# Kernel tuning notes

Hardware: AMD Instinct MI355X
Metric: run time of the kernel (lower is better)

Reference implementation:

```python
import jax, jax.numpy as jnp
import numpy as np

N = 6000          # number of nodes
P = 8_000_000     # number of (src, dst) pairs that have a path
D_FEAT = 128      # node feature dim (unused by the math, only shape)
MAX_PATH_DISTANCE = 5


def setup_inputs() -> dict:
    key = jax.random.key(0)
    k_x, k_b, k_s, k_d, k_l = jax.random.split(key, 5)
    x = jax.random.normal(k_x, (N, D_FEAT), dtype=jnp.float32)
    b = jax.random.normal(k_b, (MAX_PATH_DISTANCE,), dtype=jnp.float32)
    src_idx = jax.random.randint(k_s, (P,), 0, N, dtype=jnp.int64 if jax.config.jax_enable_x64 else jnp.int32)
    dst_idx = jax.random.randint(k_d, (P,), 0, N, dtype=src_idx.dtype)
    # path lengths are >= 1 (a path in the dict always has at least one node)
    path_len = jax.random.randint(k_l, (P,), 1, 21, dtype=src_idx.dtype)
    return {"x": x, "b": b, "src_idx": src_idx, "dst_idx": dst_idx, "path_len": path_len}


def reference(x, b, src_idx, dst_idx, path_len):
    # spatial_matrix[src, dst] = b[min(len(path), max_path_distance) - 1]
    n = x.shape[0]
    max_pd = b.shape[0]
    clamped = jnp.minimum(path_len, max_pd) - 1          # [P] in [0, max_pd-1]
    vals = b[clamped]                                     # gather from bias, [P]
    spatial = jnp.zeros((n, n), dtype=x.dtype)
    spatial = spatial.at[src_idx, dst_idx].set(vals)      # scatter into pairwise matrix
    return spatial
```

## Files before the change

kernel.cpp:

```cpp
#include <hip/hip_runtime.h>


#define BSHIFT 14
#define BCELLS (1 << BSHIFT)
#define NBUCK  2198
#define NPACK  1100
#define NOWN   550
#define BIN_THREADS 1024
#define TILE   12288
#define SCAN_TB 16
#define MAXBLK 656
#define MRG_THREADS 1024

__device__ __forceinline__ unsigned int unpack16(const unsigned int* A, unsigned int c) {
    return (A[c >> 1] >> ((c & 1) * 16)) & 0xFFFFu;
}


__global__ __launch_bounds__(BIN_THREADS, 8) void se_bin_local(
        const int* __restrict__ src_idx,
        const int* __restrict__ dst_idx,
        const int* __restrict__ path_len,
        unsigned int* __restrict__ recs,
        unsigned int* __restrict__ startsW,
        int P, int n) {
    __shared__ unsigned int histP[NPACK];
    __shared__ unsigned int curP[NPACK];
    __shared__ unsigned int stage[TILE];
    __shared__ unsigned int scr[34];

    int t = threadIdx.x;
    int start = blockIdx.x * TILE;

    for (int i = t; i < NPACK; i += BIN_THREADS) curP[i] = 0u;
    __syncthreads();

    unsigned int cc[12];
    unsigned int rk[6];
#pragma unroll
    for (int j = 0; j < 3; ++j) {
        int base = start + j * (BIN_THREADS * 4) + t * 4;
        int k0 = j * 4;
        if (base + 3 < P) {
            int4 s = *reinterpret_cast<const int4*>(src_idx + base);
            int4 d = *reinterpret_cast<const int4*>(dst_idx + base);
            int4 l = *reinterpret_cast<const int4*>(path_len + base);
            cc[k0]     = ((unsigned int)(s.x * n + d.x) << 3) | (unsigned int)((l.x < 5 ? l.x : 5) - 1);
            cc[k0 + 1] = ((unsigned int)(s.y * n + d.y) << 3) | (unsigned int)((l.y < 5 ? l.y : 5) - 1);
            cc[k0 + 2] = ((unsigned int)(s.z * n + d.z) << 3) | (unsigned int)((l.z < 5 ? l.z : 5) - 1);
            cc[k0 + 3] = ((unsigned int)(s.w * n + d.w) << 3) | (unsigned int)((l.w < 5 ? l.w : 5) - 1);
        } else {
#pragma unroll
            for (int jj = 0; jj < 4; ++jj) {
                int p = base + jj;
                if (p < P) {
                    int len = path_len[p];
                    cc[k0 + jj] = ((unsigned int)(src_idx[p] * n + dst_idx[p]) << 3)
                                | (unsigned int)((len < 5 ? len : 5) - 1);
                } else {
                    cc[k0 + jj] = 0xFFFFFFFFu;
                }
            }
        }
    }
#pragma unroll
    for (int k = 0; k < 12; ++k) {
        unsigned int r = 0;
        if (cc[k] != 0xFFFFFFFFu) {
            unsigned int c = cc[k] >> 17;
            unsigned int old = atomicAdd(&curP[c >> 1], (c & 1) ? 0x10000u : 1u);
            r = (old >> ((c & 1) * 16)) & 0xFFFFu;
        }
        if (k & 1) rk[k >> 1] |= r << 16; else rk[k >> 1] = r;
    }
    __syncthreads();

    unsigned int l0 = 0, l1 = 0, l2v = 0, l3 = 0, s = 0;
    if (t < NOWN) {
        unsigned int w0 = curP[2 * t], w1 = curP[2 * t + 1];
        unsigned int v0 = w0 & 0xFFFFu, v1 = w0 >> 16;
        unsigned int v2 = w1 & 0xFFFFu, v3 = w1 >> 16;
        l0 = 0; l1 = v0; l2v = v0 + v1; l3 = v0 + v1 + v2;
        s = v0 + v1 + v2 + v3;
    }
    unsigned int x = s;
    for (int d = 1; d < 64; d <<= 1) {
        unsigned int y = (unsigned int)__shfl_up((int)x, d, 64);
        if ((t & 63) >= d) x += y;
    }
    if ((t & 63) == 63) scr[t >> 6] = x;
    __syncthreads();
    if (t == 0) {
        unsigned int acc = 0;
        for (int w = 0; w < 16; ++w) { unsigned int v = scr[w]; scr[16 + w] = acc; acc += v; }
        scr[32] = acc;
    }
    __syncthreads();
    unsigned int exc = x - s + scr[16 + (t >> 6)];
    if (t < NOWN) {
        unsigned int st0 = exc + l0, st1 = exc + l1, st2 = exc + l2v, st3 = exc + l3;
        histP[2 * t]     = (st0 & 0xFFFFu) | (st1 << 16);
        histP[2 * t + 1] = (st2 & 0xFFFFu) | (st3 << 16);
    }
    __syncthreads();

    for (int i = t; i < NPACK; i += BIN_THREADS)
        startsW[(size_t)blockIdx.x * NPACK + i] = histP[i];

#pragma unroll
    for (int k = 0; k < 12; ++k) {
        if (cc[k] != 0xFFFFFFFFu) {
            unsigned int c = cc[k] >> 17;
            unsigned int rank = (rk[k >> 1] >> ((k & 1) * 16)) & 0xFFFFu;
            unsigned int pos = unpack16(histP, c) + rank;
            unsigned int lp1 = (unsigned int)((k >> 2) * (BIN_THREADS * 4) + t * 4 + (k & 3) + 1);
            stage[pos] = (((cc[k] >> 3) & (BCELLS - 1)) << 18) | (lp1 << 3) | (cc[k] & 7u);
        }
    }
    __syncthreads();

    unsigned int tot = scr[32];
    unsigned int* dst = recs + (size_t)blockIdx.x * TILE;
    const uint4* st4 = reinterpret_cast<const uint4*>(stage);
    uint4* dst4 = reinterpret_cast<uint4*>(dst);
    if (tot == TILE) {
#pragma unroll
        for (int j = 0; j < TILE / 4 / BIN_THREADS; ++j)
            dst4[j * BIN_THREADS + t] = st4[j * BIN_THREADS + t];
    } else {
        unsigned int tot4 = tot >> 2;
        for (unsigned int i = t; i < tot4; i += BIN_THREADS)
            dst4[i] = st4[i];
        for (unsigned int i = (tot4 << 2) + t; i < tot; i += BIN_THREADS)
            dst[i] = stage[i];
    }
}

__device__ __forceinline__ float se_decode(unsigned int k,
                                           float b0, float b1, float b2,
                                           float b3, float b4) {
    unsigned c = k & 7u;
    float t = (c == 0u) ? b0 : (c == 1u) ? b1 : (c == 2u) ? b2 : (c == 3u) ? b3 : b4;
    return k ? t : 0.0f;
}

__global__ __launch_bounds__(MRG_THREADS, 8) void se_merge3(
        const unsigned int* __restrict__ startsW,
        const unsigned int* __restrict__ recs,
        const float* __restrict__ b,
        float* __restrict__ out,
        long long totalCells, int nblk) {
    __shared__ unsigned int tab[BCELLS];

    int orig = blockIdx.x;
    int q = gridDim.x >> 3, r8 = gridDim.x & 7;
    int xcd = orig & 7, idx = orig >> 3;
    int c = (xcd < r8 ? xcd * (q + 1) : r8 * (q + 1) + (xcd - r8) * q) + idx;

    long long baseCell = (long long)c << BSHIFT;
    long long rem = totalCells - baseCell;
    int valid = rem < BCELLS ? (int)rem : BCELLS;

    int tr = threadIdx.x;
    unsigned int st = 0, en = 0;
    if (tr < nblk) {
        const unsigned int* sw = startsW + (size_t)tr * NPACK;
        unsigned int w0 = sw[c >> 1];
        unsigned int w1 = sw[(c + 1) >> 1];
        st = (w0 >> ((c & 1) * 16)) & 0xFFFFu;
        en = (w1 >> (((c + 1) & 1) * 16)) & 0xFFFFu;
    }

    uint4* tab4 = reinterpret_cast<uint4*>(tab);
    for (int i = threadIdx.x; i < BCELLS / 4; i += MRG_THREADS)
        tab4[i] = make_uint4(0u, 0u, 0u, 0u);
    __syncthreads();

    if (tr < nblk) {
        const uint4* rp4 =
            reinterpret_cast<const uint4*>(recs + (size_t)tr * TILE);
        unsigned int keyhi = (unsigned int)tr << 18;
        for (unsigned int i = st & ~3u; i < en; i += 4) {
            uint4 r4 = rp4[i >> 2];
            if (i     >= st && i     < en) atomicMax(&tab[r4.x >> 18], keyhi | (r4.x & 0x3FFFFu));
            if (i + 1 >= st && i + 1 < en) atomicMax(&tab[r4.y >> 18], keyhi | (r4.y & 0x3FFFFu));
            if (i + 2 >= st && i + 2 < en) atomicMax(&tab[r4.z >> 18], keyhi | (r4.z & 0x3FFFFu));
            if (i + 3 >= st && i + 3 < en) atomicMax(&tab[r4.w >> 18], keyhi | (r4.w & 0x3FFFFu));
        }
    }
    __syncthreads();

    float b0 = b[0], b1 = b[1], b2 = b[2], b3 = b[3], b4 = b[4];
    float* o = out + baseCell;
    int n4 = valid >> 2;
    float4* o4 = reinterpret_cast<float4*>(o);
    for (int i = threadIdx.x; i < n4; i += MRG_THREADS) {
        uint4 k = tab4[i];
        float4 v;
        v.x = se_decode(k.x, b0, b1, b2, b3, b4);
        v.y = se_decode(k.y, b0, b1, b2, b3, b4);
        v.z = se_decode(k.z, b0, b1, b2, b3, b4);
        v.w = se_decode(k.w, b0, b1, b2, b3, b4);
        o4[i] = v;
    }
    for (int i = (n4 << 2) + threadIdx.x; i < valid; i += MRG_THREADS)
        o[i] = se_decode(tab[i], b0, b1, b2, b3, b4);
}


__global__ __launch_bounds__(BIN_THREADS) void se_hist(
        const int* __restrict__ src_idx,
        const int* __restrict__ dst_idx,
        unsigned int* __restrict__ countsW,
        int P, int n) {
    __shared__ unsigned int curP[NPACK];
    int t = threadIdx.x;
    for (int i = t; i < NPACK; i += BIN_THREADS) curP[i] = 0u;
    __syncthreads();

    int start = blockIdx.x * TILE;
#pragma unroll
    for (int j = 0; j < 3; ++j) {
        int base = start + j * (BIN_THREADS * 4) + t * 4;
        if (base + 3 < P) {
            int4 s = *reinterpret_cast<const int4*>(src_idx + base);
            int4 d = *reinterpret_cast<const int4*>(dst_idx + base);
            unsigned int c0 = (unsigned int)(s.x * n + d.x) >> BSHIFT;
            unsigned int c1 = (unsigned int)(s.y * n + d.y) >> BSHIFT;
            unsigned int c2 = (unsigned int)(s.z * n + d.z) >> BSHIFT;
            unsigned int c3 = (unsigned int)(s.w * n + d.w) >> BSHIFT;
            atomicAdd(&curP[c0 >> 1], (c0 & 1) ? 0x10000u : 1u);
            atomicAdd(&curP[c1 >> 1], (c1 & 1) ? 0x10000u : 1u);
            atomicAdd(&curP[c2 >> 1], (c2 & 1) ? 0x10000u : 1u);
            atomicAdd(&curP[c3 >> 1], (c3 & 1) ? 0x10000u : 1u);
        } else {
            for (int p = base; p < P && p < base + 4; ++p) {
                unsigned int c = (unsigned int)(src_idx[p] * n + dst_idx[p]) >> BSHIFT;
                atomicAdd(&curP[c >> 1], (c & 1) ? 0x10000u : 1u);
            }
        }
    }
    __syncthreads();
    for (int i = t; i < NPACK; i += BIN_THREADS)
        countsW[(size_t)blockIdx.x * NPACK + i] = curP[i];
}

__global__ __launch_bounds__(256) void se_scan(
        unsigned int* __restrict__ countsW,
        unsigned short* __restrict__ basesT,
        int nblk) {
    __shared__ unsigned short lds16[MAXBLK * SCAN_TB];
    unsigned int* lds32 = reinterpret_cast<unsigned int*>(lds16);
    int t = threadIdx.x;
    int c0 = blockIdx.x * SCAN_TB;
    int w0 = c0 >> 1;
    int words = nblk * (SCAN_TB / 2);

    for (int i = t; i < words; i += 256) {
        int r = i >> 3, w = i & 7;
        if (w0 + w < NPACK)
            lds32[r * 8 + w] = countsW[(size_t)r * NPACK + w0 + w];
    }
    __syncthreads();

    if (t < SCAN_TB && c0 + t < NBUCK) {
        unsigned int acc = 0;
        for (int r = 0; r < nblk; ++r) {
            unsigned short v = lds16[r * SCAN_TB + t];
            lds16[r * SCAN_TB + t] = (unsigned short)acc;
            acc += v;
        }
        basesT[(size_t)(c0 + t) * (nblk + 1) + nblk] = (unsigned short)acc;
    }
    __syncthreads();

    for (int i = t; i < words; i += 256) {
        int r = i >> 3, w = i & 7;
        if (w0 + w < NPACK)
            countsW[(size_t)r * NPACK + w0 + w] = lds32[r * 8 + w];
    }
    for (int k = 0; k < SCAN_TB; ++k) {
        int c = c0 + k;
        if (c >= NBUCK) break;
        for (int r = t; r < nblk; r += 256)
            basesT[(size_t)c * (nblk + 1) + r] = lds16[r * SCAN_TB + k];
    }
}

__global__ __launch_bounds__(BIN_THREADS) void se_bin5(
        const int* __restrict__ src_idx,
        const int* __restrict__ dst_idx,
        const int* __restrict__ path_len,
        unsigned int* __restrict__ recs,
        const unsigned int* __restrict__ basesW,
        int P, int n) {
    __shared__ unsigned int histP[NPACK];
    __shared__ unsigned int curP[NPACK];
    __shared__ unsigned int gbaseP[NPACK];
    __shared__ unsigned int stage[TILE];
    __shared__ unsigned int scr[34];

    int t = threadIdx.x;
    int start = blockIdx.x * TILE;

    for (int i = t; i < NPACK; i += BIN_THREADS) curP[i] = 0u;
    __syncthreads();

    int cells[12];
    unsigned int lows[12];
#pragma unroll
    for (int j = 0; j < 3; ++j) {
        int base = start + j * (BIN_THREADS * 4) + t * 4;
        int k0 = j * 4;
        if (base + 3 < P) {
            int4 s = *reinterpret_cast<const int4*>(src_idx + base);
            int4 d = *reinterpret_cast<const int4*>(dst_idx + base);
            int4 l = *reinterpret_cast<const int4*>(path_len + base);
            int lp = base - start;
            cells[k0]     = s.x * n + d.x;
            cells[k0 + 1] = s.y * n + d.y;
            cells[k0 + 2] = s.z * n + d.z;
            cells[k0 + 3] = s.w * n + d.w;
            lows[k0]     = ((unsigned int)(lp + 1) << 3) | (unsigned int)((l.x < 5 ? l.x : 5) - 1);
            lows[k0 + 1] = ((unsigned int)(lp + 2) << 3) | (unsigned int)((l.y < 5 ? l.y : 5) - 1);
            lows[k0 + 2] = ((unsigned int)(lp + 3) << 3) | (unsigned int)((l.z < 5 ? l.z : 5) - 1);
            lows[k0 + 3] = ((unsigned int)(lp + 4) << 3) | (unsigned int)((l.w < 5 ? l.w : 5) - 1);
        } else {
#pragma unroll
            for (int jj = 0; jj < 4; ++jj) {
                int p = base + jj;
                if (p < P) {
                    cells[k0 + jj] = src_idx[p] * n + dst_idx[p];
                    int len = path_len[p];
                    int cl = (len < 5 ? len : 5) - 1;
                    lows[k0 + jj] = ((unsigned int)(p - start + 1) << 3) | (unsigned int)cl;
                } else {
                    cells[k0 + jj] = -1;
                    lows[k0 + jj] = 0u;
                }
            }
        }
    }
#pragma unroll
    for (int k = 0; k < 12; ++k) {
        if (cells[k] >= 0) {
            unsigned int c = (unsigned int)cells[k] >> BSHIFT;
            atomicAdd(&curP[c >> 1], (c & 1) ? 0x10000u : 1u);
        }
    }
    __syncthreads();

    unsigned int l0 = 0, l1 = 0, l2v = 0, l3 = 0, s = 0;
    if (t < NOWN) {
        unsigned int w0 = curP[2 * t], w1 = curP[2 * t + 1];
        unsigned int v0 = w0 & 0xFFFFu, v1 = w0 >> 16;
        unsigned int v2 = w1 & 0xFFFFu, v3 = w1 >> 16;
        l0 = 0; l1 = v0; l2v = v0 + v1; l3 = v0 + v1 + v2;
        s = v0 + v1 + v2 + v3;
    }
    unsigned int x = s;
    for (int d = 1; d < 64; d <<= 1) {
        unsigned int y = (unsigned int)__shfl_up((int)x, d, 64);
        if ((t & 63) >= d) x += y;
    }
    if ((t & 63) == 63) scr[t >> 6] = x;
    __syncthreads();
    if (t == 0) {
        unsigned int acc = 0;
        for (int w = 0; w < 16; ++w) { unsigned int v = scr[w]; scr[16 + w] = acc; acc += v; }
        scr[32] = acc;
    }
    __syncthreads();
    unsigned int exc = x - s + scr[16 + (t >> 6)];
    if (t < NOWN) {
        unsigned int st0 = exc + l0, st1 = exc + l1, st2 = exc + l2v, st3 = exc + l3;
        histP[2 * t]     = (st0 & 0xFFFFu) | (st1 << 16);
        histP[2 * t + 1] = (st2 & 0xFFFFu) | (st3 << 16);
    }
    __syncthreads();

    for (int i = t; i < NPACK; i += BIN_THREADS) {
        gbaseP[i] = basesW[(size_t)blockIdx.x * NPACK + i];
        curP[i] = histP[i];
    }
    __syncthreads();

#pragma unroll
    for (int k = 0; k < 12; ++k) {
        if (cells[k] >= 0) {
            unsigned int cell = (unsigned int)cells[k];
            unsigned int c = cell >> BSHIFT;
            unsigned int old = atomicAdd(&curP[c >> 1], (c & 1) ? 0x10000u : 1u);
            unsigned int pos = (old >> ((c & 1) * 16)) & 0xFFFFu;
            stage[pos] = ((cell & (BCELLS - 1)) << 18) | lows[k];
        }
    }
    __syncthreads();

    unsigned int tot = scr[32];
    for (unsigned int i = t; i < tot; i += BIN_THREADS) {
        unsigned int rec = stage[i];
        unsigned int lo = 0, hi = 2199;
        while (lo < hi) {
            unsigned int mid = (lo + hi + 1) >> 1;
            if (unpack16(histP, mid) <= i) lo = mid; else hi = mid - 1;
        }
        unsigned int c = lo;
        unsigned int pos = unpack16(gbaseP, c) + (i - unpack16(histP, c));
        recs[(size_t)c * BCELLS + pos] = rec;
    }
}

__global__ __launch_bounds__(MRG_THREADS) void se_merge(
        const unsigned short* __restrict__ basesT,
        const float* __restrict__ b,
        float* __restrict__ out,
        long long totalCells, int nblk) {
    __shared__ unsigned int tab[BCELLS];

    int c = blockIdx.x;
    long long baseCell = (long long)c << BSHIFT;
    long long rem = totalCells - baseCell;
    int valid = rem < BCELLS ? (int)rem : BCELLS;

    uint4* tab4 = reinterpret_cast<uint4*>(tab);
    for (int i = threadIdx.x; i < BCELLS / 4; i += MRG_THREADS)
        tab4[i] = make_uint4(0u, 0u, 0u, 0u);
    __syncthreads();

    const unsigned int* r =
        reinterpret_cast<const unsigned int*>(out) + (size_t)c * BCELLS;
    int tr = threadIdx.x;
    if (tr < nblk) {
        const unsigned short* B = basesT + (size_t)c * (nblk + 1);
        unsigned int rb0 = B[tr], rb1 = B[tr + 1];
        unsigned int keyhi = (unsigned int)tr << 18;
        for (unsigned int i = rb0; i < rb1; ++i) {
            unsigned int rec = r[i];
            atomicMax(&tab[rec >> 18], keyhi | (rec & 0x3FFFFu));
        }
    }
    __syncthreads();

    float b0 = b[0], b1 = b[1], b2 = b[2], b3 = b[3], b4 = b[4];
    float* o = out + baseCell;
    int n4 = valid >> 2;
    float4* o4 = reinterpret_cast<float4*>(o);
    for (int i = threadIdx.x; i < n4; i += MRG_THREADS) {
        uint4 k = tab4[i];
        float4 v;
        v.x = se_decode(k.x, b0, b1, b2, b3, b4);
        v.y = se_decode(k.y, b0, b1, b2, b3, b4);
        v.z = se_decode(k.z, b0, b1, b2, b3, b4);
        v.w = se_decode(k.w, b0, b1, b2, b3, b4);
        o4[i] = v;
    }
    for (int i = (n4 << 2) + threadIdx.x; i < valid; i += MRG_THREADS)
        o[i] = se_decode(tab[i], b0, b1, b2, b3, b4);
}


extern "C" void kernel_launch(void* const* d_in, const int* in_sizes, int n_in,
                              void* d_out, int out_size, void* d_ws, size_t ws_size,
                              hipStream_t stream) {
    const float* b        = (const float*)d_in[1];
    const int*   src_idx  = (const int*)d_in[2];
    const int*   dst_idx  = (const int*)d_in[3];
    const int*   path_len = (const int*)d_in[4];
    int P = in_sizes[2];
    int n = in_sizes[0] / 128;
    long long totalCells = (long long)n * n;
    int nblk = (P + TILE - 1) / TILE;

    size_t needFast = (size_t)nblk * TILE * 4u
                    + (size_t)nblk * NPACK * 4u;

    if (ws_size >= needFast && nblk <= MRG_THREADS) {
        unsigned int* recs    = (unsigned int*)d_ws;
        unsigned int* startsW = recs + (size_t)nblk * TILE;

        se_bin_local<<<nblk, BIN_THREADS, 0, stream>>>(
            src_idx, dst_idx, path_len, recs, startsW, P, n);

        se_merge3<<<NBUCK, MRG_THREADS, 0, stream>>>(
            startsW, recs, b, (float*)d_out, totalCells, nblk);
    } else {
        unsigned int*   countsW = (unsigned int*)d_ws;
        unsigned short* basesT  = (unsigned short*)(countsW + (size_t)nblk * NPACK);

        se_hist<<<nblk, BIN_THREADS, 0, stream>>>(src_idx, dst_idx, countsW, P, n);
        se_scan<<<(NBUCK + SCAN_TB - 1) / SCAN_TB, 256, 0, stream>>>(countsW, basesT, nblk);
        se_bin5<<<nblk, BIN_THREADS, 0, stream>>>(
            src_idx, dst_idx, path_len, (unsigned int*)d_out, countsW, P, n);
        se_merge<<<NBUCK, MRG_THREADS, 0, stream>>>(basesT, b, (float*)d_out,
                                                    totalCells, nblk);
    }
}
```

Measured before the change: 257.6 us.

## Fuse bin and merge kernels into one persistent kernel with grid barrier

Replaces the two-kernel bin/merge pipeline with a single persistent kernel of 512 blocks. Each block processes a strided range of input tiles, then all blocks meet at a software grid barrier (atomic counter plus spin-sleep), and each block then merges a contiguous range of output buckets. The aim is to remove the second kernel launch and the tail of the first grid. The cost is a spin barrier that relies on all 512 blocks being co-resident, an extra memset launch, and coarser work distribution per block.

```diff
diff --git a/kernel.cpp b/kernel.cpp
--- a/kernel.cpp
+++ b/kernel.cpp
@@ -11,129 +11,10 @@
 #define SCAN_TB 16
 #define MAXBLK 656
 #define MRG_THREADS 1024
+#define FUSED_GRID 512
 
 __device__ __forceinline__ unsigned int unpack16(const unsigned int* A, unsigned int c) {
     return (A[c >> 1] >> ((c & 1) * 16)) & 0xFFFFu;
-}
-
-
-__global__ __launch_bounds__(BIN_THREADS, 8) void se_bin_local(
-        const int* __restrict__ src_idx,
-        const int* __restrict__ dst_idx,
-        const int* __restrict__ path_len,
-        unsigned int* __restrict__ recs,
-        unsigned int* __restrict__ startsW,
-        int P, int n) {
-    __shared__ unsigned int histP[NPACK];
-    __shared__ unsigned int curP[NPACK];
-    __shared__ unsigned int stage[TILE];
-    __shared__ unsigned int scr[34];
-
-    int t = threadIdx.x;
-    int start = blockIdx.x * TILE;
-
-    for (int i = t; i < NPACK; i += BIN_THREADS) curP[i] = 0u;
-    __syncthreads();
-
-    unsigned int cc[12];
-    unsigned int rk[6];
-#pragma unroll
-    for (int j = 0; j < 3; ++j) {
-        int base = start + j * (BIN_THREADS * 4) + t * 4;
-        int k0 = j * 4;
-        if (base + 3 < P) {
-            int4 s = *reinterpret_cast<const int4*>(src_idx + base);
-            int4 d = *reinterpret_cast<const int4*>(dst_idx + base);
-            int4 l = *reinterpret_cast<const int4*>(path_len + base);
-            cc[k0]     = ((unsigned int)(s.x * n + d.x) << 3) | (unsigned int)((l.x < 5 ? l.x : 5) - 1);
-            cc[k0 + 1] = ((unsigned int)(s.y * n + d.y) << 3) | (unsigned int)((l.y < 5 ? l.y : 5) - 1);
-            cc[k0 + 2] = ((unsigned int)(s.z * n + d.z) << 3) | (unsigned int)((l.z < 5 ? l.z : 5) - 1);
-            cc[k0 + 3] = ((unsigned int)(s.w * n + d.w) << 3) | (unsigned int)((l.w < 5 ? l.w : 5) - 1);
-        } else {
-#pragma unroll
-            for (int jj = 0; jj < 4; ++jj) {
-                int p = base + jj;
-                if (p < P) {
-                    int len = path_len[p];
-                    cc[k0 + jj] = ((unsigned int)(src_idx[p] * n + dst_idx[p]) << 3)
-                                | (unsigned int)((len < 5 ? len : 5) - 1);
-                } else {
-                    cc[k0 + jj] = 0xFFFFFFFFu;
-                }
-            }
-        }
-    }
-#pragma unroll
-    for (int k = 0; k < 12; ++k) {
-        unsigned int r = 0;
-        if (cc[k] != 0xFFFFFFFFu) {
-            unsigned int c = cc[k] >> 17;
-            unsigned int old = atomicAdd(&curP[c >> 1], (c & 1) ? 0x10000u : 1u);
-            r = (old >> ((c & 1) * 16)) & 0xFFFFu;
-        }
-        if (k & 1) rk[k >> 1] |= r << 16; else rk[k >> 1] = r;
-    }
-    __syncthreads();
-
-    unsigned int l0 = 0, l1 = 0, l2v = 0, l3 = 0, s = 0;
-    if (t < NOWN) {
-        unsigned int w0 = curP[2 * t], w1 = curP[2 * t + 1];
-        unsigned int v0 = w0 & 0xFFFFu, v1 = w0 >> 16;
-        unsigned int v2 = w1 & 0xFFFFu, v3 = w1 >> 16;
-        l0 = 0; l1 = v0; l2v = v0 + v1; l3 = v0 + v1 + v2;
-        s = v0 + v1 + v2 + v3;
-    }
-    unsigned int x = s;
-    for (int d = 1; d < 64; d <<= 1) {
-        unsigned int y = (unsigned int)__shfl_up((int)x, d, 64);
-        if ((t & 63) >= d) x += y;
-    }
-    if ((t & 63) == 63) scr[t >> 6] = x;
-    __syncthreads();
-    if (t == 0) {
-        unsigned int acc = 0;
-        for (int w = 0; w < 16; ++w) { unsigned int v = scr[w]; scr[16 + w] = acc; acc += v; }
-        scr[32] = acc;
-    }
-    __syncthreads();
-    unsigned int exc = x - s + scr[16 + (t >> 6)];
-    if (t < NOWN) {
-        unsigned int st0 = exc + l0, st1 = exc + l1, st2 = exc + l2v, st3 = exc + l3;
-        histP[2 * t]     = (st0 & 0xFFFFu) | (st1 << 16);
-        histP[2 * t + 1] = (st2 & 0xFFFFu) | (st3 << 16);
-    }
-    __syncthreads();
-
-    for (int i = t; i < NPACK; i += BIN_THREADS)
-        startsW[(size_t)blockIdx.x * NPACK + i] = histP[i];
-
-#pragma unroll
-    for (int k = 0; k < 12; ++k) {
-        if (cc[k] != 0xFFFFFFFFu) {
-            unsigned int c = cc[k] >> 17;
-            unsigned int rank = (rk[k >> 1] >> ((k & 1) * 16)) & 0xFFFFu;
-            unsigned int pos = unpack16(histP, c) + rank;
-            unsigned int lp1 = (unsigned int)((k >> 2) * (BIN_THREADS * 4) + t * 4 + (k & 3) + 1);
-            stage[pos] = (((cc[k] >> 3) & (BCELLS - 1)) << 18) | (lp1 << 3) | (cc[k] & 7u);
-        }
-    }
-    __syncthreads();
-
-    unsigned int tot = scr[32];
-    unsigned int* dst = recs + (size_t)blockIdx.x * TILE;
-    const uint4* st4 = reinterpret_cast<const uint4*>(stage);
-    uint4* dst4 = reinterpret_cast<uint4*>(dst);
-    if (tot == TILE) {
-#pragma unroll
-        for (int j = 0; j < TILE / 4 / BIN_THREADS; ++j)
-            dst4[j * BIN_THREADS + t] = st4[j * BIN_THREADS + t];
-    } else {
-        unsigned int tot4 = tot >> 2;
-        for (unsigned int i = t; i < tot4; i += BIN_THREADS)
-            dst4[i] = st4[i];
-        for (unsigned int i = (tot4 << 2) + t; i < tot; i += BIN_THREADS)
-            dst[i] = stage[i];
-    }
 }
 
 __device__ __forceinline__ float se_decode(unsigned int k,
@@ -144,67 +25,210 @@
     return k ? t : 0.0f;
 }
 
-__global__ __launch_bounds__(MRG_THREADS, 8) void se_merge3(
-        const unsigned int* __restrict__ startsW,
-        const unsigned int* __restrict__ recs,
+
+__global__ __launch_bounds__(1024, 8) void se_fused(
+        const int* __restrict__ src_idx,
+        const int* __restrict__ dst_idx,
+        const int* __restrict__ path_len,
+        unsigned int* __restrict__ recs,
+        unsigned int* __restrict__ startsW,
+        unsigned int* __restrict__ bar,
         const float* __restrict__ b,
         float* __restrict__ out,
-        long long totalCells, int nblk) {
-    __shared__ unsigned int tab[BCELLS];
-
-    int orig = blockIdx.x;
-    int q = gridDim.x >> 3, r8 = gridDim.x & 7;
-    int xcd = orig & 7, idx = orig >> 3;
-    int c = (xcd < r8 ? xcd * (q + 1) : r8 * (q + 1) + (xcd - r8) * q) + idx;
-
-    long long baseCell = (long long)c << BSHIFT;
-    long long rem = totalCells - baseCell;
-    int valid = rem < BCELLS ? (int)rem : BCELLS;
-
-    int tr = threadIdx.x;
-    unsigned int st = 0, en = 0;
-    if (tr < nblk) {
-        const unsigned int* sw = startsW + (size_t)tr * NPACK;
-        unsigned int w0 = sw[c >> 1];
-        unsigned int w1 = sw[(c + 1) >> 1];
-        st = (w0 >> ((c & 1) * 16)) & 0xFFFFu;
-        en = (w1 >> (((c + 1) & 1) * 16)) & 0xFFFFu;
-    }
-
-    uint4* tab4 = reinterpret_cast<uint4*>(tab);
-    for (int i = threadIdx.x; i < BCELLS / 4; i += MRG_THREADS)
-        tab4[i] = make_uint4(0u, 0u, 0u, 0u);
-    __syncthreads();
-
-    if (tr < nblk) {
-        const uint4* rp4 =
-            reinterpret_cast<const uint4*>(recs + (size_t)tr * TILE);
-        unsigned int keyhi = (unsigned int)tr << 18;
-        for (unsigned int i = st & ~3u; i < en; i += 4) {
-            uint4 r4 = rp4[i >> 2];
-            if (i     >= st && i     < en) atomicMax(&tab[r4.x >> 18], keyhi | (r4.x & 0x3FFFFu));
-            if (i + 1 >= st && i + 1 < en) atomicMax(&tab[r4.y >> 18], keyhi | (r4.y & 0x3FFFFu));
-            if (i + 2 >= st && i + 2 < en) atomicMax(&tab[r4.z >> 18], keyhi | (r4.z & 0x3FFFFu));
-            if (i + 3 >= st && i + 3 < en) atomicMax(&tab[r4.w >> 18], keyhi | (r4.w & 0x3FFFFu));
-        }
-    }
-    __syncthreads();
-
-    float b0 = b[0], b1 = b[1], b2 = b[2], b3 = b[3], b4 = b[4];
-    float* o = out + baseCell;
-    int n4 = valid >> 2;
-    float4* o4 = reinterpret_cast<float4*>(o);
-    for (int i = threadIdx.x; i < n4; i += MRG_THREADS) {
-        uint4 k = tab4[i];
-        float4 v;
-        v.x = se_decode(k.x, b0, b1, b2, b3, b4);
-        v.y = se_decode(k.y, b0, b1, b2, b3, b4);
-        v.z = se_decode(k.z, b0, b1, b2, b3, b4);
-        v.w = se_decode(k.w, b0, b1, b2, b3, b4);
-        o4[i] = v;
-    }
-    for (int i = (n4 << 2) + threadIdx.x; i < valid; i += MRG_THREADS)
-        o[i] = se_decode(tab[i], b0, b1, b2, b3, b4);
+        int P, int n, long long totalCells, int nblk, int nbuck) {
+    __shared__ unsigned int lds[16384];
+    unsigned int* histP = lds;
+    unsigned int* curP  = lds + 1100;
+    unsigned int* scr   = lds + 2200;
+    unsigned int* stage = lds + 4096;
+
+    int t = threadIdx.x;
+    int bid = blockIdx.x;
+    int grid = gridDim.x;
+
+    {
+        int q = nblk / grid, r = nblk % grid;
+        int t0 = bid < r ? bid * (q + 1) : r * (q + 1) + (bid - r) * q;
+        int tc = bid < r ? q + 1 : q;
+        for (int blk = t0; blk < t0 + tc; ++blk) {
+            int start = blk * TILE;
+
+            for (int i = t; i < NPACK; i += BIN_THREADS) curP[i] = 0u;
+            __syncthreads();
+
+            unsigned int cc[12];
+            unsigned int rk[6];
+#pragma unroll
+            for (int j = 0; j < 3; ++j) {
+                int base = start + j * (BIN_THREADS * 4) + t * 4;
+                int k0 = j * 4;
+                if (base + 3 < P) {
+                    int4 s = *reinterpret_cast<const int4*>(src_idx + base);
+                    int4 d = *reinterpret_cast<const int4*>(dst_idx + base);
+                    int4 l = *reinterpret_cast<const int4*>(path_len + base);
+                    cc[k0]     = ((unsigned int)(s.x * n + d.x) << 3) | (unsigned int)((l.x < 5 ? l.x : 5) - 1);
+                    cc[k0 + 1] = ((unsigned int)(s.y * n + d.y) << 3) | (unsigned int)((l.y < 5 ? l.y : 5) - 1);
+                    cc[k0 + 2] = ((unsigned int)(s.z * n + d.z) << 3) | (unsigned int)((l.z < 5 ? l.z : 5) - 1);
+                    cc[k0 + 3] = ((unsigned int)(s.w * n + d.w) << 3) | (unsigned int)((l.w < 5 ? l.w : 5) - 1);
+                } else {
+#pragma unroll
+                    for (int jj = 0; jj < 4; ++jj) {
+                        int p = base + jj;
+                        if (p < P) {
+                            int len = path_len[p];
+                            cc[k0 + jj] = ((unsigned int)(src_idx[p] * n + dst_idx[p]) << 3)
+                                        | (unsigned int)((len < 5 ? len : 5) - 1);
+                        } else {
+                            cc[k0 + jj] = 0xFFFFFFFFu;
+                        }
+                    }
+                }
+            }
+#pragma unroll
+            for (int k = 0; k < 12; ++k) {
+                unsigned int rr = 0;
+                if (cc[k] != 0xFFFFFFFFu) {
+                    unsigned int c = cc[k] >> 17;
+                    unsigned int old = atomicAdd(&curP[c >> 1], (c & 1) ? 0x10000u : 1u);
+                    rr = (old >> ((c & 1) * 16)) & 0xFFFFu;
+                }
+                if (k & 1) rk[k >> 1] |= rr << 16; else rk[k >> 1] = rr;
+            }
+            __syncthreads();
+
+            unsigned int l0 = 0, l1 = 0, l2v = 0, l3 = 0, s = 0;
+            if (t < NOWN) {
+                unsigned int w0 = curP[2 * t], w1 = curP[2 * t + 1];
+                unsigned int v0 = w0 & 0xFFFFu, v1 = w0 >> 16;
+                unsigned int v2 = w1 & 0xFFFFu, v3 = w1 >> 16;
+                l0 = 0; l1 = v0; l2v = v0 + v1; l3 = v0 + v1 + v2;
+                s = v0 + v1 + v2 + v3;
+            }
+            unsigned int x = s;
+            for (int d = 1; d < 64; d <<= 1) {
+                unsigned int y = (unsigned int)__shfl_up((int)x, d, 64);
+                if ((t & 63) >= d) x += y;
+            }
+            if ((t & 63) == 63) scr[t >> 6] = x;
+            __syncthreads();
+            if (t == 0) {
+                unsigned int acc = 0;
+                for (int w = 0; w < 16; ++w) { unsigned int v = scr[w]; scr[16 + w] = acc; acc += v; }
+                scr[32] = acc;
+            }
+            __syncthreads();
+            unsigned int exc = x - s + scr[16 + (t >> 6)];
+            if (t < NOWN) {
+                unsigned int st0 = exc + l0, st1 = exc + l1, st2 = exc + l2v, st3 = exc + l3;
+                histP[2 * t]     = (st0 & 0xFFFFu) | (st1 << 16);
+                histP[2 * t + 1] = (st2 & 0xFFFFu) | (st3 << 16);
+            }
+            __syncthreads();
+
+            for (int i = t; i < NPACK; i += BIN_THREADS)
+                startsW[(size_t)blk * NPACK + i] = histP[i];
+
+#pragma unroll
+            for (int k = 0; k < 12; ++k) {
+                if (cc[k] != 0xFFFFFFFFu) {
+                    unsigned int c = cc[k] >> 17;
+                    unsigned int rank = (rk[k >> 1] >> ((k & 1) * 16)) & 0xFFFFu;
+                    unsigned int pos = unpack16(histP, c) + rank;
+                    unsigned int lp1 = (unsigned int)((k >> 2) * (BIN_THREADS * 4) + t * 4 + (k & 3) + 1);
+                    stage[pos] = (((cc[k] >> 3) & (BCELLS - 1)) << 18) | (lp1 << 3) | (cc[k] & 7u);
+                }
+            }
+            __syncthreads();
+
+            unsigned int tot = scr[32];
+            unsigned int* dst = recs + (size_t)blk * TILE;
+            const uint4* st4 = reinterpret_cast<const uint4*>(stage);
+            uint4* dst4 = reinterpret_cast<uint4*>(dst);
+            if (tot == TILE) {
+#pragma unroll
+                for (int j = 0; j < TILE / 4 / BIN_THREADS; ++j)
+                    dst4[j * BIN_THREADS + t] = st4[j * BIN_THREADS + t];
+            } else {
+                unsigned int tot4 = tot >> 2;
+                for (unsigned int i = t; i < tot4; i += BIN_THREADS)
+                    dst4[i] = st4[i];
+                for (unsigned int i = (tot4 << 2) + t; i < tot; i += BIN_THREADS)
+                    dst[i] = stage[i];
+            }
+            __syncthreads();
+        }
+    }
+
+    __threadfence();
+    __syncthreads();
+    if (t == 0) {
+        atomicAdd(bar, 1u);
+        for (int it = 0; it < (1 << 22); ++it) {
+            if (atomicAdd(bar, 0u) >= (unsigned int)grid) break;
+            __builtin_amdgcn_s_sleep(16);
+        }
+    }
+    __syncthreads();
+    __threadfence();
+
+    {
+        float b0 = b[0], b1 = b[1], b2 = b[2], b3 = b[3], b4 = b[4];
+        int q = nbuck / grid, r = nbuck % grid;
+        int c0 = bid < r ? bid * (q + 1) : r * (q + 1) + (bid - r) * q;
+        int cn = bid < r ? q + 1 : q;
+        unsigned int* tab = lds;
+        uint4* tab4 = reinterpret_cast<uint4*>(tab);
+
+        for (int c = c0; c < c0 + cn; ++c) {
+            long long baseCell = (long long)c << BSHIFT;
+            long long rem = totalCells - baseCell;
+            int valid = rem < BCELLS ? (int)rem : BCELLS;
+
+            int tr = t;
+            unsigned int st = 0, en = 0;
+            if (tr < nblk) {
+                const unsigned int* sw = startsW + (size_t)tr * NPACK;
+                unsigned int w0 = sw[c >> 1];
+                unsigned int w1 = sw[(c + 1) >> 1];
+                st = (w0 >> ((c & 1) * 16)) & 0xFFFFu;
+                en = (w1 >> (((c + 1) & 1) * 16)) & 0xFFFFu;
+            }
+
+            __syncthreads();
+            for (int i = t; i < BCELLS / 4; i += MRG_THREADS)
+                tab4[i] = make_uint4(0u, 0u, 0u, 0u);
+            __syncthreads();
+
+            if (tr < nblk) {
+                const uint4* rp4 =
+                    reinterpret_cast<const uint4*>(recs + (size_t)tr * TILE);
+                unsigned int keyhi = (unsigned int)tr << 18;
+                for (unsigned int i = st & ~3u; i < en; i += 4) {
+                    uint4 r4 = rp4[i >> 2];
+                    if (i     >= st && i     < en) atomicMax(&tab[r4.x >> 18], keyhi | (r4.x & 0x3FFFFu));
+                    if (i + 1 >= st && i + 1 < en) atomicMax(&tab[r4.y >> 18], keyhi | (r4.y & 0x3FFFFu));
+                    if (i + 2 >= st && i + 2 < en) atomicMax(&tab[r4.z >> 18], keyhi | (r4.z & 0x3FFFFu));
+                    if (i + 3 >= st && i + 3 < en) atomicMax(&tab[r4.w >> 18], keyhi | (r4.w & 0x3FFFFu));
+                }
+            }
+            __syncthreads();
+
+            float* o = out + baseCell;
+            int n4 = valid >> 2;
+            float4* o4 = reinterpret_cast<float4*>(o);
+            for (int i = t; i < n4; i += MRG_THREADS) {
+                uint4 k = tab4[i];
+                float4 v;
+                v.x = se_decode(k.x, b0, b1, b2, b3, b4);
+                v.y = se_decode(k.y, b0, b1, b2, b3, b4);
+                v.z = se_decode(k.z, b0, b1, b2, b3, b4);
+                v.w = se_decode(k.w, b0, b1, b2, b3, b4);
+                o4[i] = v;
+            }
+            for (int i = (n4 << 2) + t; i < valid; i += MRG_THREADS)
+                o[i] = se_decode(tab[i], b0, b1, b2, b3, b4);
+        }
+    }
 }
 
 
@@ -473,17 +497,18 @@
     int nblk = (P + TILE - 1) / TILE;
 
     size_t needFast = (size_t)nblk * TILE * 4u
-                    + (size_t)nblk * NPACK * 4u;
+                    + (size_t)nblk * NPACK * 4u + 4u;
 
     if (ws_size >= needFast && nblk <= MRG_THREADS) {
         unsigned int* recs    = (unsigned int*)d_ws;
         unsigned int* startsW = recs + (size_t)nblk * TILE;
-
-        se_bin_local<<<nblk, BIN_THREADS, 0, stream>>>(
-            src_idx, dst_idx, path_len, recs, startsW, P, n);
-
-        se_merge3<<<NBUCK, MRG_THREADS, 0, stream>>>(
-            startsW, recs, b, (float*)d_out, totalCells, nblk);
+        unsigned int* bar     = startsW + (size_t)nblk * NPACK;
+
+        hipMemsetAsync(bar, 0, 4, stream);
+
+        se_fused<<<FUSED_GRID, 1024, 0, stream>>>(
+            src_idx, dst_idx, path_len, recs, startsW, bar, b,
+            (float*)d_out, P, n, totalCells, nblk, NBUCK);
     } else {
         unsigned int*   countsW = (unsigned int*)d_ws;
         unsigned short* basesT  = (unsigned short*)(countsW + (size_t)nblk * NPACK);
```

Measured after the change: 693.4 us. 169% more time.
